# Optimization experiments

Hardware: AMD Instinct MI355X
Metric: run time of the kernel (lower is better)

## Reference

```python
import jax, jax.numpy as jnp
import numpy as np

N = 4_000_000
D = 8
NEG = jnp.float32(-1e30)  # finite stand-in for -inf to keep grads NaN-free
MT_W, RMAV_W, RANK_W = 0.5, 0.1, 0.3


def setup_inputs() -> dict:
    key = jax.random.key(0)
    k1, k2, k3, k4 = jax.random.split(key, 4)
    pred = jax.random.normal(k1, (N, D), dtype=jnp.float32)
    target = jax.random.uniform(k2, (N, D), dtype=jnp.float32)
    mask = jax.random.randint(k3, (N,), 0, 2).astype(bool)
    rmav_target = jax.random.uniform(k4, (N, D), dtype=jnp.float32)
    return {"pred": pred, "target": target, "mask": mask, "rmav_target": rmav_target}


def _listmle(scores, targets, mask):
    # sort descending by target; masked-out rows pushed to the tail
    key_t = jnp.where(mask, targets, NEG)
    order = jnp.argsort(-key_t)
    s = scores[order]                      # [N]
    m = mask[order]                        # [N]
    s_m = jnp.where(m, s, NEG)
    # reverse cumulative logsumexp == the original python loop, parallelized
    cum = jax.lax.cumlogsumexp(s_m, axis=0, reverse=True)
    lp = jnp.where(m, s - cum, 0.0)
    cnt = mask.sum().astype(scores.dtype)
    return -lp.sum() / cnt


def reference(pred, target, mask, rmav_target):
    mf = mask.astype(pred.dtype)           # [N]
    cnt = mf.sum()
    k = pred.shape[1] - 1                  # aux task count
    # masked MSE on composite column
    loss_composite = ((pred[:, 0] - target[:, 0]) ** 2 * mf).sum() / cnt
    # masked MSE on aux columns (mean over masked rows x k cols)
    loss_multitask = (((pred[:, 1:] - target[:, 1:]) ** 2) * mf[:, None]).sum() / (cnt * k)
    # ListMLE ranking loss on composite scores of labeled rows
    loss_ranking = _listmle(pred[:, 0], target[:, 0], mask)
    supervised = loss_composite + MT_W * loss_multitask + RANK_W * loss_ranking
    # RMAV consistency on unlabeled rows, aux columns
    umf = 1.0 - mf
    ucnt = umf.sum()
    loss_cons = (((pred[:, 1:] - rmav_target[:, 1:]) ** 2) * umf[:, None]).sum() / (ucnt * k)
    total = supervised + RMAV_W * loss_cons
    return total, loss_composite, loss_multitask, loss_ranking, loss_cons
```

## Files before the change

### kernel.cpp

```cpp
#include <hip/hip_runtime.h>
#include <math.h>


#define NB 65536
#define MAXCAP 96
#define SUMB 1024

#define OFF_MAIN   128
#define OFF_RANK   (OFF_MAIN + 5*64*8)
#define OFF_BPART  (OFF_RANK + 256*8)
#define OFF_BBASE  (OFF_BPART + SUMB*8)
#define OFF_BCOUNT (OFF_BBASE + SUMB*8)
#define OFF_BSUM   (OFF_BCOUNT + NB*4)
#define OFF_SLOTS  (OFF_BSUM + NB*8)

__global__ void zero_ws(unsigned int* __restrict__ w, int nwords) {
    int i = blockIdx.x * blockDim.x + threadIdx.x;
    if (i < nwords) w[i] = 0u;
}

__global__ __launch_bounds__(256)
void main_pass(const float4* __restrict__ pred,
               const float4* __restrict__ tgt,
               const float4* __restrict__ rmav,
               const void* __restrict__ maskp,
               int N, int CAP,
               int* __restrict__ bcount,
               float2* __restrict__ slots,
               double* __restrict__ pm)
{
    bool bytemode;
    {
        const unsigned int* mw = (const unsigned int*)maskp;
        int nw = N >> 2; if (nw > 64) nw = 64; if (nw < 1) nw = 1;
        int lane = threadIdx.x & 63;
        unsigned int v = (lane < nw) ? mw[lane] : 0u;
        bytemode = (__ballot(v > 1u) != 0ull);
    }
    const unsigned char* m8 = (const unsigned char*)maskp;
    const int* m32 = (const int*)maskp;

    double comp = 0.0, mt = 0.0, cons = 0.0, ssum = 0.0;
    int cntl = 0;
    const int tid = blockIdx.x * blockDim.x + threadIdx.x;
    const int S = gridDim.x * blockDim.x;

    for (int i0 = tid; i0 < N; i0 += 4 * S) {
        int   bk[4];
        float ek[4], key[4];
        #pragma unroll
        for (int k = 0; k < 4; k++) {
            bk[k] = -1;
            int i = i0 + k * S;
            if (i >= N) continue;
            bool m = bytemode ? (m8[i] != 0) : (m32[i] != 0);
            float4 pa = pred[2 * i];
            float4 pb = pred[2 * i + 1];
            if (m) {
                float4 ta = tgt[2 * i];
                float4 tb = tgt[2 * i + 1];
                float d0 = pa.x - ta.x;
                comp += (double)(d0 * d0);
                float s1 = (pa.y - ta.y) * (pa.y - ta.y)
                         + (pa.z - ta.z) * (pa.z - ta.z)
                         + (pa.w - ta.w) * (pa.w - ta.w);
                float s2 = (pb.x - tb.x) * (pb.x - tb.x)
                         + (pb.y - tb.y) * (pb.y - tb.y)
                         + (pb.z - tb.z) * (pb.z - tb.z)
                         + (pb.w - tb.w) * (pb.w - tb.w);
                mt += (double)(s1 + s2);
                ssum += (double)pa.x;
                cntl++;
                if (CAP > 0) {
                    ek[k]  = expf(pa.x);
                    key[k] = ta.x;
                    int b = (int)(ta.x * 65536.0f);
                    bk[k] = b < 0 ? 0 : (b > NB - 1 ? NB - 1 : b);
                }
            } else {
                float4 ra = rmav[2 * i];
                float4 rb = rmav[2 * i + 1];
                float s1 = (pa.y - ra.y) * (pa.y - ra.y)
                         + (pa.z - ra.z) * (pa.z - ra.z)
                         + (pa.w - ra.w) * (pa.w - ra.w);
                float s2 = (pb.x - rb.x) * (pb.x - rb.x)
                         + (pb.y - rb.y) * (pb.y - rb.y)
                         + (pb.z - rb.z) * (pb.z - rb.z)
                         + (pb.w - rb.w) * (pb.w - rb.w);
                cons += (double)(s1 + s2);
            }
        }
        int pos[4];
        #pragma unroll
        for (int k = 0; k < 4; k++)
            if (bk[k] >= 0) pos[k] = atomicAdd(&bcount[bk[k]], 1);
        #pragma unroll
        for (int k = 0; k < 4; k++)
            if (bk[k] >= 0 && pos[k] < CAP)
                slots[(size_t)bk[k] * CAP + pos[k]] = make_float2(key[k], ek[k]);
    }

    for (int off = 32; off > 0; off >>= 1) {
        comp += __shfl_down(comp, off, 64);
        mt   += __shfl_down(mt,   off, 64);
        cons += __shfl_down(cons, off, 64);
        ssum += __shfl_down(ssum, off, 64);
        cntl += __shfl_down(cntl, off, 64);
    }
    __shared__ double sred[4][5];
    int wave = threadIdx.x >> 6, lane = threadIdx.x & 63;
    if (lane == 0) {
        sred[wave][0] = comp; sred[wave][1] = mt; sred[wave][2] = cons;
        sred[wave][3] = ssum; sred[wave][4] = (double)cntl;
    }
    __syncthreads();
    if (threadIdx.x == 0) {
        double a0 = 0, a1 = 0, a2 = 0, a3 = 0, a4 = 0;
        for (int w = 0; w < 4; w++) {
            a0 += sred[w][0]; a1 += sred[w][1]; a2 += sred[w][2];
            a3 += sred[w][3]; a4 += sred[w][4];
        }
        int slot = blockIdx.x & 63;
        atomicAdd(&pm[0 * 64 + slot], a0);
        atomicAdd(&pm[1 * 64 + slot], a1);
        atomicAdd(&pm[2 * 64 + slot], a2);
        atomicAdd(&pm[3 * 64 + slot], a3);
        atomicAdd(&pm[4 * 64 + slot], a4);
    }
}

__global__ __launch_bounds__(256)
void bucket_sum_partial(const int* __restrict__ bcount, const float2* __restrict__ slots,
                        int CAP, double* __restrict__ bsum, double* __restrict__ bpart)
{
    int wave = threadIdx.x >> 6, lane = threadIdx.x & 63;
    int b0 = blockIdx.x * 64 + wave * 16;
    double wtot = 0.0;
    for (int q = 0; q < 16; q++) {
        int b = b0 + q;
        int n = bcount[b]; if (n > CAP) n = CAP;
        const float2* sl = slots + (size_t)b * CAP;
        double s = 0.0;
        for (int i = lane; i < n; i += 64) s += (double)sl[i].y;
        for (int off = 32; off > 0; off >>= 1) s += __shfl_down(s, off, 64);
        if (lane == 0) { bsum[b] = s; wtot += s; }
    }
    __shared__ double wred[4];
    if (lane == 0) wred[wave] = wtot;
    __syncthreads();
    if (threadIdx.x == 0)
        bpart[blockIdx.x] = wred[0] + wred[1] + wred[2] + wred[3];
}

__global__ __launch_bounds__(256)
void scan_partials(const double* __restrict__ bpart, double* __restrict__ bbase)
{
    __shared__ double lds[256];
    int t = threadIdx.x;
    double v0 = bpart[4 * t], v1 = bpart[4 * t + 1],
           v2 = bpart[4 * t + 2], v3 = bpart[4 * t + 3];
    double s = v0 + v1 + v2 + v3;
    lds[t] = s;
    __syncthreads();
    for (int off = 1; off < 256; off <<= 1) {
        double u = (t >= off) ? lds[t - off] : 0.0;
        __syncthreads();
        lds[t] += u;
        __syncthreads();
    }
    double base = lds[t] - s;
    bbase[4 * t] = base; base += v0;
    bbase[4 * t + 1] = base; base += v1;
    bbase[4 * t + 2] = base; base += v2;
    bbase[4 * t + 3] = base;
}

__global__ __launch_bounds__(64)
void apply_scan(double* __restrict__ bsum, const double* __restrict__ bbase)
{
    int lane = threadIdx.x;
    int b = blockIdx.x * 64 + lane;
    double s = bsum[b];
    double x = s;
    for (int off = 1; off < 64; off <<= 1) {
        double u = __shfl_up(x, off, 64);
        if (lane >= off) x += u;
    }
    bsum[b] = bbase[blockIdx.x] + x - s;
}

__global__ __launch_bounds__(256)
void bucket_rank(const int* __restrict__ bcount, const float2* __restrict__ slots,
                 const double* __restrict__ btail, int CAP,
                 double* __restrict__ pr)
{
    int lane = threadIdx.x & 63;
    int wave = threadIdx.x >> 6;
    int b = blockIdx.x * 4 + wave;
    double a = 0.0;
    if (b < NB) {
        int n = bcount[b]; if (n > CAP) n = CAP;
        if (n > 0) {
            double tail = btail[b];
            const float2* sl = slots + (size_t)b * CAP;
            for (int i = lane; i < n; i += 64) {
                float2 ei = sl[i];
                double local = 0.0;
                for (int j = 0; j < n; j++) {
                    float2 ej = sl[j];
                    bool after = (ej.x < ei.x) || (ej.x == ei.x && j > i);
                    if (after) local += (double)ej.y;
                }
                double T = tail + (double)ei.y + local;
                a += (double)logf((float)T);
            }
        }
    }
    for (int off = 32; off > 0; off >>= 1) a += __shfl_down(a, off, 64);
    __shared__ double sred[4];
    if (lane == 0) sred[wave] = a;
    __syncthreads();
    if (threadIdx.x == 0) {
        double s = sred[0] + sred[1] + sred[2] + sred[3];
        atomicAdd(&pr[blockIdx.x & 255], s);
    }
}

__global__ void finalize(const double* __restrict__ pm, const double* __restrict__ pr,
                         float* __restrict__ out, int N)
{
    int lane = threadIdx.x;
    double q0 = pm[0 * 64 + lane];
    double q1 = pm[1 * 64 + lane];
    double q2 = pm[2 * 64 + lane];
    double q3 = pm[3 * 64 + lane];
    double q4 = pm[4 * 64 + lane];
    double r  = pr[lane] + pr[lane + 64] + pr[lane + 128] + pr[lane + 192];
    for (int off = 32; off > 0; off >>= 1) {
        q0 += __shfl_down(q0, off, 64);
        q1 += __shfl_down(q1, off, 64);
        q2 += __shfl_down(q2, off, 64);
        q3 += __shfl_down(q3, off, 64);
        q4 += __shfl_down(q4, off, 64);
        r  += __shfl_down(r,  off, 64);
    }
    if (lane == 0) {
        double cnt  = q4;
        double comp = q0 / cnt;
        double mt   = q1 / (cnt * 7.0);
        double ucnt = (double)N - cnt;
        double cons = q2 / (ucnt * 7.0);
        double rank = (r - q3) / cnt;
        double total = comp + 0.5 * mt + 0.3 * rank + 0.1 * cons;
        out[0] = (float)total;
        out[1] = (float)comp;
        out[2] = (float)mt;
        out[3] = (float)rank;
        out[4] = (float)cons;
    }
}

extern "C" void kernel_launch(void* const* d_in, const int* in_sizes, int n_in,
                              void* d_out, int out_size, void* d_ws, size_t ws_size,
                              hipStream_t stream) {
    const float* pred = (const float*)d_in[0];
    const float* tgt  = (const float*)d_in[1];
    const void* maskp = d_in[2];
    const float* rmav = (const float*)d_in[3];
    const int N = in_sizes[2];

    char* ws = (char*)d_ws;
    double* pm     = (double*)(ws + OFF_MAIN);
    double* pr     = (double*)(ws + OFF_RANK);
    double* bpart  = (double*)(ws + OFF_BPART);
    double* bbase  = (double*)(ws + OFF_BBASE);
    int*    bcount = (int*)(ws + OFF_BCOUNT);
    double* bsum   = (double*)(ws + OFF_BSUM);
    float2* slots  = (float2*)(ws + OFF_SLOTS);

    size_t avail = (ws_size > (size_t)OFF_SLOTS) ? (ws_size - (size_t)OFF_SLOTS) : 0;
    int CAP = (int)(avail / ((size_t)NB * sizeof(float2)));
    if (CAP > MAXCAP) CAP = MAXCAP;
    if (CAP < 0) CAP = 0;
    const bool have_buckets = (CAP > 0);

    size_t zbytes = (size_t)OFF_BSUM;
    if (zbytes > ws_size) zbytes = ws_size;
    int zwords = (int)(zbytes / 4);
    if (zwords > 0)
        zero_ws<<<(zwords + 255) / 256, 256, 0, stream>>>((unsigned int*)ws, zwords);
    if (ws_size < (size_t)OFF_BCOUNT) return;

    main_pass<<<4096, 256, 0, stream>>>(
        (const float4*)pred, (const float4*)tgt, (const float4*)rmav,
        maskp, N, have_buckets ? CAP : 0, bcount, slots, pm);

    if (have_buckets) {
        bucket_sum_partial<<<SUMB, 256, 0, stream>>>(bcount, slots, CAP, bsum, bpart);
        scan_partials<<<1, 256, 0, stream>>>(bpart, bbase);
        apply_scan<<<SUMB, 64, 0, stream>>>(bsum, bbase);
        bucket_rank<<<NB / 4, 256, 0, stream>>>(bcount, slots, bsum, CAP, pr);
    }
    finalize<<<1, 64, 0, stream>>>(pm, pr, (float*)d_out, N);
}
```

Measured before the change: 511.8 us.

## Fuse bucket tail kernels into one cooperative kernel and software-pipeline slot stores

Replaces the four post-pass kernels (bucket sum, scan, apply scan, rank, finalize) with a single cooperative kernel that uses grid-wide syncs, with the old launch chain kept as a fallback if the cooperative launch fails. The main pass drops its 4-way unrolled loop and instead issues each row's bucket atomic immediately, deferring that row's slot store to the next iteration to hide the atomic's latency. The aim is to cut kernel-launch gaps and tail overhead. The cooperative launch requires all 1024 blocks to be co-resident, and the rank stage now runs on 1024 blocks instead of 16384, which gives it less parallelism; the main loop also loses its memory-level parallelism from unrolling.

```diff
diff --git a/kernel.cpp b/kernel.cpp
--- a/kernel.cpp
+++ b/kernel.cpp
@@ -1,5 +1,8 @@
 #include <hip/hip_runtime.h>
+#include <hip/hip_cooperative_groups.h>
 #include <math.h>
+
+namespace cg = cooperative_groups;
 
 
 #define NB 65536
@@ -45,60 +48,52 @@
     const int tid = blockIdx.x * blockDim.x + threadIdx.x;
     const int S = gridDim.x * blockDim.x;
 
-    for (int i0 = tid; i0 < N; i0 += 4 * S) {
-        int   bk[4];
-        float ek[4], key[4];
-        #pragma unroll
-        for (int k = 0; k < 4; k++) {
-            bk[k] = -1;
-            int i = i0 + k * S;
-            if (i >= N) continue;
-            bool m = bytemode ? (m8[i] != 0) : (m32[i] != 0);
-            float4 pa = pred[2 * i];
-            float4 pb = pred[2 * i + 1];
-            if (m) {
-                float4 ta = tgt[2 * i];
-                float4 tb = tgt[2 * i + 1];
-                float d0 = pa.x - ta.x;
-                comp += (double)(d0 * d0);
-                float s1 = (pa.y - ta.y) * (pa.y - ta.y)
-                         + (pa.z - ta.z) * (pa.z - ta.z)
-                         + (pa.w - ta.w) * (pa.w - ta.w);
-                float s2 = (pb.x - tb.x) * (pb.x - tb.x)
-                         + (pb.y - tb.y) * (pb.y - tb.y)
-                         + (pb.z - tb.z) * (pb.z - tb.z)
-                         + (pb.w - tb.w) * (pb.w - tb.w);
-                mt += (double)(s1 + s2);
-                ssum += (double)pa.x;
-                cntl++;
-                if (CAP > 0) {
-                    ek[k]  = expf(pa.x);
-                    key[k] = ta.x;
-                    int b = (int)(ta.x * 65536.0f);
-                    bk[k] = b < 0 ? 0 : (b > NB - 1 ? NB - 1 : b);
-                }
-            } else {
-                float4 ra = rmav[2 * i];
-                float4 rb = rmav[2 * i + 1];
-                float s1 = (pa.y - ra.y) * (pa.y - ra.y)
-                         + (pa.z - ra.z) * (pa.z - ra.z)
-                         + (pa.w - ra.w) * (pa.w - ra.w);
-                float s2 = (pb.x - rb.x) * (pb.x - rb.x)
-                         + (pb.y - rb.y) * (pb.y - rb.y)
-                         + (pb.z - rb.z) * (pb.z - rb.z)
-                         + (pb.w - rb.w) * (pb.w - rb.w);
-                cons += (double)(s1 + s2);
+    int   pbk = -1, ppos = 0;
+    float pkey = 0.0f, pe = 0.0f;
+
+    for (int i = tid; i < N; i += S) {
+        bool m = bytemode ? (m8[i] != 0) : (m32[i] != 0);
+        float4 pa = pred[2 * i];
+        float4 pb = pred[2 * i + 1];
+        if (m) {
+            float4 ta = tgt[2 * i];
+            float4 tb = tgt[2 * i + 1];
+            float d0 = pa.x - ta.x;
+            comp += (double)(d0 * d0);
+            float s1 = (pa.y - ta.y) * (pa.y - ta.y)
+                     + (pa.z - ta.z) * (pa.z - ta.z)
+                     + (pa.w - ta.w) * (pa.w - ta.w);
+            float s2 = (pb.x - tb.x) * (pb.x - tb.x)
+                     + (pb.y - tb.y) * (pb.y - tb.y)
+                     + (pb.z - tb.z) * (pb.z - tb.z)
+                     + (pb.w - tb.w) * (pb.w - tb.w);
+            mt += (double)(s1 + s2);
+            ssum += (double)pa.x;
+            cntl++;
+            if (CAP > 0) {
+                float e = expf(pa.x);
+                int b = (int)(ta.x * 65536.0f);
+                b = b < 0 ? 0 : (b > NB - 1 ? NB - 1 : b);
+                int pos = atomicAdd(&bcount[b], 1);
+                if (pbk >= 0 && ppos < CAP)
+                    slots[(size_t)pbk * CAP + ppos] = make_float2(pkey, pe);
+                pbk = b; ppos = pos; pkey = ta.x; pe = e;
             }
-        }
-        int pos[4];
-        #pragma unroll
-        for (int k = 0; k < 4; k++)
-            if (bk[k] >= 0) pos[k] = atomicAdd(&bcount[bk[k]], 1);
-        #pragma unroll
-        for (int k = 0; k < 4; k++)
-            if (bk[k] >= 0 && pos[k] < CAP)
-                slots[(size_t)bk[k] * CAP + pos[k]] = make_float2(key[k], ek[k]);
-    }
+        } else {
+            float4 ra = rmav[2 * i];
+            float4 rb = rmav[2 * i + 1];
+            float s1 = (pa.y - ra.y) * (pa.y - ra.y)
+                     + (pa.z - ra.z) * (pa.z - ra.z)
+                     + (pa.w - ra.w) * (pa.w - ra.w);
+            float s2 = (pb.x - rb.x) * (pb.x - rb.x)
+                     + (pb.y - rb.y) * (pb.y - rb.y)
+                     + (pb.z - rb.z) * (pb.z - rb.z)
+                     + (pb.w - rb.w) * (pb.w - rb.w);
+            cons += (double)(s1 + s2);
+        }
+    }
+    if (pbk >= 0 && ppos < CAP)
+        slots[(size_t)pbk * CAP + ppos] = make_float2(pkey, pe);
 
     for (int off = 32; off > 0; off >>= 1) {
         comp += __shfl_down(comp, off, 64);
@@ -126,6 +121,131 @@
         atomicAdd(&pm[2 * 64 + slot], a2);
         atomicAdd(&pm[3 * 64 + slot], a3);
         atomicAdd(&pm[4 * 64 + slot], a4);
+    }
+}
+
+__global__ __launch_bounds__(256, 4)
+void tail_coop(const int* __restrict__ bcount, const float2* __restrict__ slots,
+               int CAP,
+               double* __restrict__ bsum, double* __restrict__ bpart,
+               double* __restrict__ bbase,
+               const double* __restrict__ pm, double* __restrict__ pr,
+               float* __restrict__ out, int N)
+{
+    cg::grid_group grid = cg::this_grid();
+    const int t = threadIdx.x, wave = t >> 6, lane = t & 63;
+    const int blk = blockIdx.x;
+
+    __shared__ double wred[4];
+    __shared__ double scan_lds[256];
+    __shared__ double tail_lds[64];
+
+    const int b0 = blk * 64 + wave * 16;
+    double wtot = 0.0;
+    for (int q = 0; q < 16; q++) {
+        int b = b0 + q;
+        int n = bcount[b]; if (n > CAP) n = CAP;
+        const float2* sl = slots + (size_t)b * CAP;
+        double s = 0.0;
+        for (int i = lane; i < n; i += 64) s += (double)sl[i].y;
+        for (int off = 32; off > 0; off >>= 1) s += __shfl_down(s, off, 64);
+        if (lane == 0) { bsum[b] = s; wtot += s; }
+    }
+    if (lane == 0) wred[wave] = wtot;
+    __syncthreads();
+    if (t == 0) bpart[blk] = wred[0] + wred[1] + wred[2] + wred[3];
+    grid.sync();
+
+    if (blk == 0) {
+        double v0 = bpart[4 * t], v1 = bpart[4 * t + 1],
+               v2 = bpart[4 * t + 2], v3 = bpart[4 * t + 3];
+        double s = v0 + v1 + v2 + v3;
+        scan_lds[t] = s;
+        __syncthreads();
+        for (int off = 1; off < 256; off <<= 1) {
+            double u = (t >= off) ? scan_lds[t - off] : 0.0;
+            __syncthreads();
+            scan_lds[t] += u;
+            __syncthreads();
+        }
+        double base = scan_lds[t] - s;
+        bbase[4 * t] = base; base += v0;
+        bbase[4 * t + 1] = base; base += v1;
+        bbase[4 * t + 2] = base; base += v2;
+        bbase[4 * t + 3] = base;
+    }
+    grid.sync();
+
+    if (wave == 0) {
+        double s = bsum[blk * 64 + lane];
+        double x = s;
+        for (int off = 1; off < 64; off <<= 1) {
+            double u = __shfl_up(x, off, 64);
+            if (lane >= off) x += u;
+        }
+        tail_lds[lane] = bbase[blk] + x - s;
+    }
+    __syncthreads();
+
+    double a = 0.0;
+    for (int q = 0; q < 16; q++) {
+        int b = b0 + q;
+        int n = bcount[b]; if (n > CAP) n = CAP;
+        if (n > 0) {
+            double tail = tail_lds[wave * 16 + q];
+            const float2* sl = slots + (size_t)b * CAP;
+            for (int i = lane; i < n; i += 64) {
+                float2 ei = sl[i];
+                double local = 0.0;
+                for (int j = 0; j < n; j++) {
+                    float2 ej = sl[j];
+                    bool after = (ej.x < ei.x) || (ej.x == ei.x && j > i);
+                    if (after) local += (double)ej.y;
+                }
+                double T = tail + (double)ei.y + local;
+                a += (double)logf((float)T);
+            }
+        }
+    }
+    for (int off = 32; off > 0; off >>= 1) a += __shfl_down(a, off, 64);
+    __syncthreads();
+    if (lane == 0) wred[wave] = a;
+    __syncthreads();
+    if (t == 0) {
+        double s = wred[0] + wred[1] + wred[2] + wred[3];
+        atomicAdd(&pr[blk & 255], s);
+    }
+    grid.sync();
+
+    if (blk == 0 && wave == 0) {
+        double q0 = pm[0 * 64 + lane];
+        double q1 = pm[1 * 64 + lane];
+        double q2 = pm[2 * 64 + lane];
+        double q3 = pm[3 * 64 + lane];
+        double q4 = pm[4 * 64 + lane];
+        double r  = pr[lane] + pr[lane + 64] + pr[lane + 128] + pr[lane + 192];
+        for (int off = 32; off > 0; off >>= 1) {
+            q0 += __shfl_down(q0, off, 64);
+            q1 += __shfl_down(q1, off, 64);
+            q2 += __shfl_down(q2, off, 64);
+            q3 += __shfl_down(q3, off, 64);
+            q4 += __shfl_down(q4, off, 64);
+            r  += __shfl_down(r,  off, 64);
+        }
+        if (lane == 0) {
+            double cnt  = q4;
+            double comp = q0 / cnt;
+            double mtv  = q1 / (cnt * 7.0);
+            double ucnt = (double)N - cnt;
+            double cons = q2 / (ucnt * 7.0);
+            double rank = (r - q3) / cnt;
+            double total = comp + 0.5 * mtv + 0.3 * rank + 0.1 * cons;
+            out[0] = (float)total;
+            out[1] = (float)comp;
+            out[2] = (float)mtv;
+            out[3] = (float)rank;
+            out[4] = (float)cons;
+        }
     }
 }
 
@@ -145,11 +265,10 @@
         for (int off = 32; off > 0; off >>= 1) s += __shfl_down(s, off, 64);
         if (lane == 0) { bsum[b] = s; wtot += s; }
     }
-    __shared__ double wred[4];
-    if (lane == 0) wred[wave] = wtot;
-    __syncthreads();
-    if (threadIdx.x == 0)
-        bpart[blockIdx.x] = wred[0] + wred[1] + wred[2] + wred[3];
+    __shared__ double wr[4];
+    if (lane == 0) wr[wave] = wtot;
+    __syncthreads();
+    if (threadIdx.x == 0) bpart[blockIdx.x] = wr[0] + wr[1] + wr[2] + wr[3];
 }
 
 __global__ __launch_bounds__(256)
@@ -296,10 +415,21 @@
         maskp, N, have_buckets ? CAP : 0, bcount, slots, pm);
 
     if (have_buckets) {
-        bucket_sum_partial<<<SUMB, 256, 0, stream>>>(bcount, slots, CAP, bsum, bpart);
-        scan_partials<<<1, 256, 0, stream>>>(bpart, bbase);
-        apply_scan<<<SUMB, 64, 0, stream>>>(bsum, bbase);
-        bucket_rank<<<NB / 4, 256, 0, stream>>>(bcount, slots, bsum, CAP, pr);
-    }
-    finalize<<<1, 64, 0, stream>>>(pm, pr, (float*)d_out, N);
-}
+        float* outp = (float*)d_out;
+        int cap = CAP, n = N;
+        void* args[] = { (void*)&bcount, (void*)&slots, (void*)&cap,
+                         (void*)&bsum, (void*)&bpart, (void*)&bbase,
+                         (void*)&pm, (void*)&pr, (void*)&outp, (void*)&n };
+        hipError_t err = hipLaunchCooperativeKernel(
+            (const void*)tail_coop, dim3(SUMB), dim3(256), args, 0, stream);
+        if (err != hipSuccess) {
+            bucket_sum_partial<<<SUMB, 256, 0, stream>>>(bcount, slots, CAP, bsum, bpart);
+            scan_partials<<<1, 256, 0, stream>>>(bpart, bbase);
+            apply_scan<<<SUMB, 64, 0, stream>>>(bsum, bbase);
+            bucket_rank<<<NB / 4, 256, 0, stream>>>(bcount, slots, bsum, CAP, pr);
+            finalize<<<1, 64, 0, stream>>>(pm, pr, (float*)d_out, N);
+        }
+    } else {
+        finalize<<<1, 64, 0, stream>>>(pm, pr, (float*)d_out, N);
+    }
+}
```

After: 817.4 us. 59.7% more time.
